# Kernel tuning notes

Hardware: AMD Instinct MI355X
Metric: run time of the kernel (lower is better)

The kernel has to match this reference:

```python
import jax, jax.numpy as jnp
import numpy as np

B, D_IN, D_H, D_OUT = 8192, 512, 256, 128
TEMP = 0.07
EPS_BN = 1e-5


def _bn(x, g, b):
    # BatchNorm1d in training mode: biased batch statistics
    mu = jnp.mean(x, axis=0)
    var = jnp.var(x, axis=0)
    return (x - mu) * jax.lax.rsqrt(var + EPS_BN) * g + b


def _project(x, W1, b1, g1, beta1, W2, b2, g2, beta2, W3, b3):
    h = jax.nn.relu(_bn(x @ W1 + b1, g1, beta1))
    h = jax.nn.relu(_bn(h @ W2 + b2, g2, beta2))
    return h @ W3 + b3  # (B, D_OUT)


def setup_inputs() -> dict:
    key = jax.random.key(0)
    ks = jax.random.split(key, 6)
    f32 = jnp.float32
    return {
        "x1": jax.random.normal(ks[0], (B, D_IN), f32),
        "x2": jax.random.normal(ks[1], (B, D_IN), f32),
        "W1": jax.random.normal(ks[2], (D_IN, D_H), f32) * 0.04,
        "b1": jnp.zeros((D_H,), f32),
        "g1": jnp.ones((D_H,), f32),
        "beta1": jnp.zeros((D_H,), f32),
        "W2": jax.random.normal(ks[3], (D_H, D_H), f32) * 0.06,
        "b2": jnp.zeros((D_H,), f32),
        "g2": jnp.ones((D_H,), f32),
        "beta2": jnp.zeros((D_H,), f32),
        "W3": jax.random.normal(ks[4], (D_H, D_OUT), f32) * 0.06,
        "b3": jnp.zeros((D_OUT,), f32),
    }


def reference(x1, x2, W1, b1, g1, beta1, W2, b2, g2, beta2, W3, b3):
    z1 = _project(x1, W1, b1, g1, beta1, W2, b2, g2, beta2, W3, b3)
    z2 = _project(x2, W1, b1, g1, beta1, W2, b2, g2, beta2, W3, b3)
    # F.normalize(dim=1), eps=1e-12
    z1 = z1 / jnp.maximum(jnp.linalg.norm(z1, axis=1, keepdims=True), 1e-12)
    z2 = z2 / jnp.maximum(jnp.linalg.norm(z2, axis=1, keepdims=True), 1e-12)
    reps = jnp.concatenate([z1, z2], axis=0)           # (2B, D)
    # cosine similarity of unit vectors == single GEMM (2B, 2B)
    sim = reps @ reps.T
    idx = jnp.arange(B)
    positives = jnp.concatenate([sim[idx, idx + B], sim[idx + B, idx]], axis=0)  # (2B,)
    nominator = jnp.exp(positives / TEMP)
    # source bug preserved: denominator sums sim/temp (no exp), masking the diagonal
    denominator = (jnp.sum(sim, axis=1) - jnp.diagonal(sim)) / TEMP
    loss = -jnp.log(nominator / denominator)
    return jnp.mean(loss)
```

## Files before the change

kernel.cpp:

```cpp
#include <hip/hip_runtime.h>
#include <math.h>

#define BATCH   8192
#define MROWS   16384
#define DIN     512
#define DH      256
#define DOUT    128
#define EPS_BN  1e-5f
#define TEMP    0.07f

using f4    = __attribute__((ext_vector_type(4))) float;
using f32x4 = __attribute__((ext_vector_type(4))) float;
using h4    = __attribute__((ext_vector_type(4))) _Float16;
using h8    = __attribute__((ext_vector_type(8))) _Float16;

#define GLD_LDS16(gp, lp) __builtin_amdgcn_global_load_lds( \
    (const __attribute__((address_space(1))) void*)(gp),    \
    (__attribute__((address_space(3))) void*)(lp), 16, 0, 0)


template <int K, int N, int EPI>
__global__ __launch_bounds__(256, 1) void gemm3h(
    const _Float16* __restrict__ Ahi, const _Float16* __restrict__ Alo,
    const _Float16* __restrict__ BThi, const _Float16* __restrict__ BTlo,
    const float* __restrict__ bias, float* __restrict__ Cout,
    float* __restrict__ red)
{
    constexpr int BM = 64, BN = 128;
    constexpr int NT = K / 64;
    constexpr int TA = 4096, TB = 8192;
    constexpr int BUF = 24576;

    __shared__ _Float16 ring[3][BUF];

    const int tid = threadIdx.x;
    const int wave = tid >> 6, lane = tid & 63;
    const int wr = wave >> 1, wc = wave & 1;
    const int l4 = lane >> 4, lc = lane & 15;
    const int brow = blockIdx.y * BM;
    const int bcol = blockIdx.x * BN;
    const size_t aT0 = (size_t)(brow >> 6) * NT;
    const size_t bT0 = (size_t)(bcol >> 7) * NT;

    const _Float16* srcb[12];
    int str[12];
#pragma unroll
    for (int i = 0; i < 12; ++i) {
        int c = wave * 12 + i;
        if (c < 8)       { srcb[i] = Ahi  + aT0 * TA + c * 512;        str[i] = TA; }
        else if (c < 16) { srcb[i] = Alo  + aT0 * TA + (c - 8) * 512;  str[i] = TA; }
        else if (c < 32) { srcb[i] = BThi + bT0 * TB + (c - 16) * 512; str[i] = TB; }
        else             { srcb[i] = BTlo + bT0 * TB + (c - 32) * 512; str[i] = TB; }
        srcb[i] += lane * 8;
    }

    auto stage = [&](int buf, int t) {
#pragma unroll
        for (int i = 0; i < 12; ++i)
            GLD_LDS16(srcb[i] + (size_t)t * str[i], &ring[buf][(wave * 12 + i) * 512]);
    };

    f32x4 acc[2][4];
#pragma unroll
    for (int mi = 0; mi < 2; ++mi)
#pragma unroll
        for (int ni = 0; ni < 4; ++ni)
#pragma unroll
            for (int c = 0; c < 4; ++c) acc[mi][ni][c] = 0.f;

    stage(0, 0);
    stage(1, 1);

#pragma unroll
    for (int t = 0; t < NT; ++t) {
        if (t < NT - 1) asm volatile("s_waitcnt vmcnt(12)" ::: "memory");
        else            asm volatile("s_waitcnt vmcnt(0)" ::: "memory");
        __builtin_amdgcn_s_barrier();
        __builtin_amdgcn_sched_barrier(0);
        const _Float16* L = ring[t % 3];
#pragma unroll
        for (int ks = 0; ks < 2; ++ks) {
            h8 ah[2], al[2], bh[4], bl[4];
#pragma unroll
            for (int mi = 0; mi < 2; ++mi) {
                int mf = wr * 2 + mi;
                ah[mi] = *(const h8*)&L[(mf * 2 + ks) * 512 + lane * 8];
                al[mi] = *(const h8*)&L[(8 + mf * 2 + ks) * 512 + lane * 8];
            }
#pragma unroll
            for (int ni = 0; ni < 4; ++ni) {
                int nf = wc * 4 + ni;
                bh[ni] = *(const h8*)&L[(16 + nf * 2 + ks) * 512 + lane * 8];
                bl[ni] = *(const h8*)&L[(32 + nf * 2 + ks) * 512 + lane * 8];
            }
#pragma unroll
            for (int mi = 0; mi < 2; ++mi)
#pragma unroll
                for (int ni = 0; ni < 4; ++ni) {
                    acc[mi][ni] = __builtin_amdgcn_mfma_f32_16x16x32_f16(
                        ah[mi], bh[ni], acc[mi][ni], 0, 0, 0);
                    acc[mi][ni] = __builtin_amdgcn_mfma_f32_16x16x32_f16(
                        al[mi], bh[ni], acc[mi][ni], 0, 0, 0);
                    acc[mi][ni] = __builtin_amdgcn_mfma_f32_16x16x32_f16(
                        ah[mi], bl[ni], acc[mi][ni], 0, 0, 0);
                }
        }
        if (t + 2 < NT) stage((t + 2) % 3, t + 2);
    }

    __syncthreads();
    float* sR = (float*)&ring[0][0];
    float* nL = (float*)((char*)sR + 8192);

    float bv[4];
#pragma unroll
    for (int ni = 0; ni < 4; ++ni) bv[ni] = bias[bcol + wc * 64 + ni * 16 + lc];

    if constexpr (EPI == 0) {
        const int half = (brow >= BATCH) ? 1 : 0;
        float s[4] = {}, q[4] = {};
#pragma unroll
        for (int mi = 0; mi < 2; ++mi)
#pragma unroll
            for (int j = 0; j < 4; ++j) {
                int gr = brow + wr * 32 + mi * 16 + l4 * 4 + j;
#pragma unroll
                for (int ni = 0; ni < 4; ++ni) {
                    float v = acc[mi][ni][j] + bv[ni];
                    Cout[(size_t)gr * N + bcol + wc * 64 + ni * 16 + lc] = v;
                    s[ni] += v;
                    q[ni] = fmaf(v, v, q[ni]);
                }
            }
#pragma unroll
        for (int ni = 0; ni < 4; ++ni) {
            sR[(wr * 4 + l4) * 128 + wc * 64 + ni * 16 + lc] = s[ni];
            sR[1024 + (wr * 4 + l4) * 128 + wc * 64 + ni * 16 + lc] = q[ni];
        }
        __syncthreads();
        if (tid < BN) {
            float ss = 0.f, qq = 0.f;
#pragma unroll
            for (int i = 0; i < 8; ++i) {
                ss += sR[i * 128 + tid];
                qq += sR[1024 + i * 128 + tid];
            }
            atomicAdd(&red[half * 512 + bcol + tid], ss);
            atomicAdd(&red[half * 512 + 256 + bcol + tid], qq);
        }
    } else {
        float v[2][4][4];
#pragma unroll
        for (int mi = 0; mi < 2; ++mi)
#pragma unroll
            for (int j = 0; j < 4; ++j) {
                float ssq = 0.f;
#pragma unroll
                for (int ni = 0; ni < 4; ++ni) {
                    v[mi][j][ni] = acc[mi][ni][j] + bv[ni];
                    ssq = fmaf(v[mi][j][ni], v[mi][j][ni], ssq);
                }
#pragma unroll
                for (int o = 1; o < 16; o <<= 1) ssq += __shfl_xor(ssq, o);
                if (lc == 0) nL[(wr * 32 + mi * 16 + l4 * 4 + j) * 2 + wc] = ssq;
            }
        __syncthreads();
        float s[4] = {};
#pragma unroll
        for (int mi = 0; mi < 2; ++mi)
#pragma unroll
            for (int j = 0; j < 4; ++j) {
                int lrow = wr * 32 + mi * 16 + l4 * 4 + j;
                float tot = nL[lrow * 2] + nL[lrow * 2 + 1];
                float inv = 1.0f / fmaxf(sqrtf(tot), 1e-12f);
#pragma unroll
                for (int ni = 0; ni < 4; ++ni) {
                    float z = v[mi][j][ni] * inv;
                    Cout[(size_t)(brow + lrow) * DOUT + wc * 64 + ni * 16 + lc] = z;
                    s[ni] += z;
                }
            }
        __syncthreads();
#pragma unroll
        for (int ni = 0; ni < 4; ++ni)
            sR[(wr * 4 + l4) * 128 + wc * 64 + ni * 16 + lc] = s[ni];
        __syncthreads();
        if (tid < BN) {
            float ss = 0.f;
#pragma unroll
            for (int i = 0; i < 8; ++i) ss += sR[i * 128 + tid];
            atomicAdd(&red[tid], ss);
        }
    }
}

__device__ __forceinline__ size_t tiledA(int r, int k, int KT) {
    return (size_t)((r >> 6) * KT + (k >> 6)) * 4096 +
           ((((r & 63) >> 4) * 2 + ((k & 63) >> 5)) * 512) +
           (((r & 15) | (((k & 31) >> 3) << 4)) * 8) + (k & 7);
}
__device__ __forceinline__ size_t tiledB(int n, int k, int KT) {
    return (size_t)((n >> 7) * KT + (k >> 6)) * 8192 +
           ((((n & 127) >> 4) * 2 + ((k & 63) >> 5)) * 512) +
           (((n & 15) | (((k & 31) >> 3) << 4)) * 8) + (k & 7);
}

__global__ __launch_bounds__(256) void split_xw(
    const float* __restrict__ x1, const float* __restrict__ x2,
    const float* __restrict__ W1, const float* __restrict__ W2,
    const float* __restrict__ W3,
    _Float16* __restrict__ Xhi, _Float16* __restrict__ Xlo,
    _Float16* __restrict__ W1hiT, _Float16* __restrict__ W1loT,
    _Float16* __restrict__ W2hiT, _Float16* __restrict__ W2loT,
    _Float16* __restrict__ W3hiT, _Float16* __restrict__ W3loT)
{
    const int b = blockIdx.x;
    if (b < 2048) {
        const float* src = (b < 1024) ? x1 : x2;
        const int rbase = (b < 1024) ? 0 : BATCH;
#pragma unroll
        for (int i = 0; i < 4; ++i) {
            size_t f = (size_t)(b & 1023) * 1024 + i * 256 + threadIdx.x;
            int r = rbase + (int)(f >> 7);
            int c0 = ((int)f & 127) << 2;
            f4 vv = ((const f4*)src)[f];
            h4 hi, lo;
#pragma unroll
            for (int j = 0; j < 4; ++j) {
                hi[j] = (_Float16)vv[j];
                lo[j] = (_Float16)(vv[j] - (float)hi[j]);
            }
            size_t d = tiledA(r, c0, DIN / 64);
            *(h4*)&Xhi[d] = hi;
            *(h4*)&Xlo[d] = lo;
        }
    } else {
        const int wb = b - 2048;
#pragma unroll
        for (int i = 0; i < 4; ++i) {
            int e = wb * 1024 + i * 256 + threadIdx.x;
            if (e < 131072) {
                int n = e >> 9, k = e & 511;
                float w = W1[(size_t)k * 256 + n];
                _Float16 hi = (_Float16)w;
                size_t d = tiledB(n, k, 8);
                W1hiT[d] = hi; W1loT[d] = (_Float16)(w - (float)hi);
            } else if (e < 196608) {
                int r = e - 131072;
                int n = r >> 8, k = r & 255;
                float w = W2[(size_t)k * 256 + n];
                _Float16 hi = (_Float16)w;
                size_t d = tiledB(n, k, 4);
                W2hiT[d] = hi; W2loT[d] = (_Float16)(w - (float)hi);
            } else {
                int r = e - 196608;
                int n = r >> 8, k = r & 255;
                float w = W3[(size_t)k * 128 + n];
                _Float16 hi = (_Float16)w;
                size_t d = tiledB(n, k, 4);
                W3hiT[d] = hi; W3loT[d] = (_Float16)(w - (float)hi);
            }
        }
    }
}

__global__ __launch_bounds__(256) void bnrelu_split(
    const float* __restrict__ Y, const float* __restrict__ stats,
    const float* __restrict__ g, const float* __restrict__ beta,
    _Float16* __restrict__ Hhi, _Float16* __restrict__ Hlo)
{
    const int c0 = (threadIdx.x & 63) << 2;
    const int rj = threadIdx.x >> 6;
    const int row0 = blockIdx.x * 64;
    const int half = (row0 >= BATCH) ? 1 : 0;
    const float invN = 1.0f / (float)BATCH;
    f4 sc, sh;
#pragma unroll
    for (int j = 0; j < 4; ++j) {
        int c = c0 + j;
        float mu = stats[half * 512 + c] * invN;
        float var = fmaf(-mu, mu, stats[half * 512 + 256 + c] * invN);
        float s = g[c] * rsqrtf(var + EPS_BN);
        sc[j] = s;
        sh[j] = fmaf(-mu, s, beta[c]);
    }
#pragma unroll 4
    for (int it = 0; it < 16; ++it) {
        int row = row0 + it * 4 + rj;
        f4 v = *(const f4*)(Y + (size_t)row * DH + c0);
        h4 hi, lo;
#pragma unroll
        for (int j = 0; j < 4; ++j) {
            float h = fmaxf(fmaf(v[j], sc[j], sh[j]), 0.f);
            hi[j] = (_Float16)h;
            lo[j] = (_Float16)(h - (float)hi[j]);
        }
        size_t d = tiledA(row, c0, DH / 64);
        *(h4*)&Hhi[d] = hi;
        *(h4*)&Hlo[d] = lo;
    }
}

__global__ __launch_bounds__(256) void losspos(const float* __restrict__ reps,
                                               const float* __restrict__ Svec,
                                               float* __restrict__ out)
{
    const int lane = threadIdx.x & 63;
    const int grp = threadIdx.x >> 6;
    __shared__ float part[4];
    float2 sv = ((const float2*)Svec)[lane];
    float acc = 0.f;
#pragma unroll 1
    for (int it = 0; it < 8; ++it) {
        int p = blockIdx.x * 32 + it * 4 + grp;
        float2 a = ((const float2*)(reps + (size_t)p * DOUT))[lane];
        float2 b = ((const float2*)(reps + (size_t)(p + BATCH) * DOUT))[lane];
        float dp  = fmaf(a.x, b.x, a.y * b.y);
        float rsA = fmaf(a.x, sv.x, a.y * sv.y);
        float sdA = fmaf(a.x, a.x, a.y * a.y);
        float rsB = fmaf(b.x, sv.x, b.y * sv.y);
        float sdB = fmaf(b.x, b.x, b.y * b.y);
#pragma unroll
        for (int o = 32; o; o >>= 1) {
            dp  += __shfl_xor(dp, o);
            rsA += __shfl_xor(rsA, o);
            sdA += __shfl_xor(sdA, o);
            rsB += __shfl_xor(rsB, o);
            sdB += __shfl_xor(sdB, o);
        }
        if (lane == 0) {
            float nom = expf(dp / TEMP);
            float dA = (rsA - sdA) / TEMP;
            float dB = (rsB - sdB) / TEMP;
            acc += -logf(nom / dA) - logf(nom / dB);
        }
    }
    if (lane == 0) part[grp] = acc;
    __syncthreads();
    if (threadIdx.x == 0) {
        float t = part[0] + part[1] + part[2] + part[3];
        atomicAdd(out, t * (1.0f / (float)MROWS));
    }
}

__global__ void zero_kernel(float* __restrict__ smalls, float* __restrict__ out)
{
    int i = blockIdx.x * 256 + threadIdx.x;
    if (i < 2176) smalls[i] = 0.f;
    if (i == 0) out[0] = 0.f;
}

extern "C" void kernel_launch(void* const* d_in, const int* in_sizes, int n_in,
                              void* d_out, int out_size, void* d_ws, size_t ws_size,
                              hipStream_t stream)
{
    const float* x1    = (const float*)d_in[0];
    const float* x2    = (const float*)d_in[1];
    const float* W1    = (const float*)d_in[2];
    const float* b1    = (const float*)d_in[3];
    const float* g1    = (const float*)d_in[4];
    const float* beta1 = (const float*)d_in[5];
    const float* W2    = (const float*)d_in[6];
    const float* b2    = (const float*)d_in[7];
    const float* g2    = (const float*)d_in[8];
    const float* beta2 = (const float*)d_in[9];
    const float* W3    = (const float*)d_in[10];
    const float* b3    = (const float*)d_in[11];
    float* out = (float*)d_out;

    char* W = (char*)d_ws;
    _Float16* XHI  = (_Float16*)(W);
    _Float16* XLO  = (_Float16*)(W + (16u << 20));
    float*    Y1   = (float*)   (W + (32u << 20));
    _Float16* H1HI = (_Float16*)(W);
    _Float16* H1LO = (_Float16*)(W + (8u << 20));
    float*    Y2   = (float*)   (W + (16u << 20));
    _Float16* H2HI = (_Float16*)(W);
    _Float16* H2LO = (_Float16*)(W + (8u << 20));
    float*    REPS = (float*)   (W + (16u << 20));
    char* wb = W + (48u << 20);
    _Float16* W1HIT = (_Float16*)(wb);
    _Float16* W1LOT = (_Float16*)(wb + 262144);
    _Float16* W2HIT = (_Float16*)(wb + 524288);
    _Float16* W2LOT = (_Float16*)(wb + 655360);
    _Float16* W3HIT = (_Float16*)(wb + 786432);
    _Float16* W3LOT = (_Float16*)(wb + 851968);
    float* smalls   = (float*)  (wb + 917504);
    float* stats1 = smalls;
    float* stats2 = smalls + 1024;
    float* Svec   = smalls + 2048;

    zero_kernel<<<9, 256, 0, stream>>>(smalls, out);

    split_xw<<<2272, 256, 0, stream>>>(x1, x2, W1, W2, W3, XHI, XLO,
                                       W1HIT, W1LOT, W2HIT, W2LOT, W3HIT, W3LOT);

    gemm3h<DIN, DH, 0><<<dim3(DH / 128, MROWS / 64), 256, 0, stream>>>(
        XHI, XLO, W1HIT, W1LOT, b1, Y1, stats1);
    bnrelu_split<<<MROWS / 64, 256, 0, stream>>>(Y1, stats1, g1, beta1, H1HI, H1LO);

    gemm3h<DH, DH, 0><<<dim3(DH / 128, MROWS / 64), 256, 0, stream>>>(
        H1HI, H1LO, W2HIT, W2LOT, b2, Y2, stats2);
    bnrelu_split<<<MROWS / 64, 256, 0, stream>>>(Y2, stats2, g2, beta2, H2HI, H2LO);

    gemm3h<DH, DOUT, 1><<<dim3(DOUT / 128, MROWS / 64), 256, 0, stream>>>(
        H2HI, H2LO, W3HIT, W3LOT, b3, REPS, Svec);

    losspos<<<BATCH / 32, 256, 0, stream>>>(REPS, Svec, out);
}
```

Before: 190.6 us.

## Fuse fp16 split and BatchNorm+ReLU into GEMM A-operand loading

The GEMM kernel now reads fp32 activations directly from global memory, applies the previous layer's BatchNorm scale/shift and ReLU in registers, and splits values into hi/lo fp16 before writing them to LDS. The standalone input split pass and the two bnrelu_split kernels go away, along with their tiled fp16 intermediate buffers. Weight prep and zeroing are merged into one small kernel. The K-step drops to 32 with a register-prefetched A path and launch bounds raised to 2 blocks per CU, which trades extra VALU conversion work inside the GEMM loop for less HBM traffic and fewer launches.

```diff
diff --git a/kernel.cpp b/kernel.cpp
--- a/kernel.cpp
+++ b/kernel.cpp
@@ -18,48 +18,87 @@
     (const __attribute__((address_space(1))) void*)(gp),    \
     (__attribute__((address_space(3))) void*)(lp), 16, 0, 0)
 
-
-template <int K, int N, int EPI>
-__global__ __launch_bounds__(256, 1) void gemm3h(
-    const _Float16* __restrict__ Ahi, const _Float16* __restrict__ Alo,
+template <int K, int N, int FUSE_BN, int EPI>
+__global__ __launch_bounds__(256, 2) void gemm_fused(
+    const float* __restrict__ A1, const float* __restrict__ A2, int splitRow,
     const _Float16* __restrict__ BThi, const _Float16* __restrict__ BTlo,
-    const float* __restrict__ bias, float* __restrict__ Cout,
-    float* __restrict__ red)
+    const float* __restrict__ stats, const float* __restrict__ g,
+    const float* __restrict__ beta, const float* __restrict__ bias,
+    float* __restrict__ Cout, float* __restrict__ red)
 {
-    constexpr int BM = 64, BN = 128;
-    constexpr int NT = K / 64;
-    constexpr int TA = 4096, TB = 8192;
-    constexpr int BUF = 24576;
-
-    __shared__ _Float16 ring[3][BUF];
+    constexpr int NT = K / 32;
 
     const int tid = threadIdx.x;
     const int wave = tid >> 6, lane = tid & 63;
     const int wr = wave >> 1, wc = wave & 1;
     const int l4 = lane >> 4, lc = lane & 15;
-    const int brow = blockIdx.y * BM;
-    const int bcol = blockIdx.x * BN;
-    const size_t aT0 = (size_t)(brow >> 6) * NT;
-    const size_t bT0 = (size_t)(bcol >> 7) * NT;
-
-    const _Float16* srcb[12];
-    int str[12];
-#pragma unroll
-    for (int i = 0; i < 12; ++i) {
-        int c = wave * 12 + i;
-        if (c < 8)       { srcb[i] = Ahi  + aT0 * TA + c * 512;        str[i] = TA; }
-        else if (c < 16) { srcb[i] = Alo  + aT0 * TA + (c - 8) * 512;  str[i] = TA; }
-        else if (c < 32) { srcb[i] = BThi + bT0 * TB + (c - 16) * 512; str[i] = TB; }
-        else             { srcb[i] = BTlo + bT0 * TB + (c - 32) * 512; str[i] = TB; }
-        srcb[i] += lane * 8;
-    }
-
-    auto stage = [&](int buf, int t) {
-#pragma unroll
-        for (int i = 0; i < 12; ++i)
-            GLD_LDS16(srcb[i] + (size_t)t * str[i], &ring[buf][(wave * 12 + i) * 512]);
+    const int wg = blockIdx.x;
+    const int brow = (wg & 255) * 64;
+    const int bcol = (wg >> 8) * 128;
+    const int half = (brow >= BATCH) ? 1 : 0;
+
+    __shared__ __align__(16) char smem[75776];
+    _Float16* Bring = (_Float16*)smem;
+    _Float16* Aring = (_Float16*)(smem + 49152);
+    float*    scsh  = (float*)(smem + 73728);
+    float*    sR    = (float*)(smem + 49152);
+    float*    nLp   = (float*)(smem + 49152 + 8192);
+
+    const _Float16* bsrc[4];
+    {
+        const int co = (bcol + wave * 32 + lc) * K + l4 * 8;
+        bsrc[0] = BThi + co;
+        bsrc[1] = BThi + co + 16 * K;
+        bsrc[2] = BTlo + co;
+        bsrc[3] = BTlo + co + 16 * K;
+    }
+    auto stageB = [&](int buf, int t) {
+        _Float16* d = Bring + buf * 8192 + wave * 1024;
+        GLD_LDS16(bsrc[0] + t * 32, d);
+        GLD_LDS16(bsrc[1] + t * 32, d + 512);
+        GLD_LDS16(bsrc[2] + t * 32, d + 4096);
+        GLD_LDS16(bsrc[3] + t * 32, d + 4096 + 512);
     };
 
+    const int arow = wave * 16 + lc;
+    const int ak0 = l4 * 8;
+    const int growA = brow + arow;
+    const float* asrc = (growA < splitRow)
+        ? (A1 + (size_t)growA * K + ak0)
+        : (A2 + (size_t)(growA - splitRow) * K + ak0);
+
+    f4 ar[2][2];
+    auto loadA = [&](int p, int t) {
+        ar[p][0] = *(const f4*)(asrc + t * 32);
+        ar[p][1] = *(const f4*)(asrc + t * 32 + 4);
+    };
+    auto procA = [&](int p, int buf, int t) {
+        float v[8];
+#pragma unroll
+        for (int j = 0; j < 4; ++j) { v[j] = ar[p][0][j]; v[4 + j] = ar[p][1][j]; }
+        if constexpr (FUSE_BN) {
+            f4 s0 = *(const f4*)&scsh[t * 32 + ak0];
+            f4 s1 = *(const f4*)&scsh[t * 32 + ak0 + 4];
+            f4 h0 = *(const f4*)&scsh[256 + t * 32 + ak0];
+            f4 h1 = *(const f4*)&scsh[256 + t * 32 + ak0 + 4];
+#pragma unroll
+            for (int j = 0; j < 4; ++j) {
+                v[j]     = fmaxf(fmaf(v[j],     s0[j], h0[j]), 0.f);
+                v[4 + j] = fmaxf(fmaf(v[4 + j], s1[j], h1[j]), 0.f);
+            }
+        }
+        h8 hi, lo;
+#pragma unroll
+        for (int j = 0; j < 8; ++j) {
+            _Float16 h = (_Float16)v[j];
+            hi[j] = h;
+            lo[j] = (_Float16)(v[j] - (float)h);
+        }
+        _Float16* d = Aring + buf * 4096 + wave * 512 + lane * 8;
+        *(h8*)d = hi;
+        *(h8*)(d + 2048) = lo;
+    };
+
     f32x4 acc[2][4];
 #pragma unroll
     for (int mi = 0; mi < 2; ++mi)
@@ -68,56 +107,75 @@
 #pragma unroll
             for (int c = 0; c < 4; ++c) acc[mi][ni][c] = 0.f;
 
-    stage(0, 0);
-    stage(1, 1);
+    auto compute = [&](int buf) {
+        const _Float16* Ab = Aring + buf * 4096;
+        const _Float16* Bb = Bring + buf * 8192;
+        h8 ah[2], al[2], bh[4], bl[4];
+#pragma unroll
+        for (int mi = 0; mi < 2; ++mi) {
+            ah[mi] = *(const h8*)(Ab + (wr * 2 + mi) * 512 + lane * 8);
+            al[mi] = *(const h8*)(Ab + 2048 + (wr * 2 + mi) * 512 + lane * 8);
+        }
+#pragma unroll
+        for (int ni = 0; ni < 4; ++ni) {
+            bh[ni] = *(const h8*)(Bb + (wc * 4 + ni) * 512 + lane * 8);
+            bl[ni] = *(const h8*)(Bb + 4096 + (wc * 4 + ni) * 512 + lane * 8);
+        }
+#pragma unroll
+        for (int mi = 0; mi < 2; ++mi)
+#pragma unroll
+            for (int ni = 0; ni < 4; ++ni) {
+                acc[mi][ni] = __builtin_amdgcn_mfma_f32_16x16x32_f16(
+                    ah[mi], bh[ni], acc[mi][ni], 0, 0, 0);
+                acc[mi][ni] = __builtin_amdgcn_mfma_f32_16x16x32_f16(
+                    al[mi], bh[ni], acc[mi][ni], 0, 0, 0);
+                acc[mi][ni] = __builtin_amdgcn_mfma_f32_16x16x32_f16(
+                    ah[mi], bl[ni], acc[mi][ni], 0, 0, 0);
+            }
+    };
+
+    if constexpr (FUSE_BN) {
+        const float invN = 1.0f / (float)BATCH;
+        float mu = stats[half * 512 + tid] * invN;
+        float var = fmaf(-mu, mu, stats[half * 512 + 256 + tid] * invN);
+        float s = g[tid] * rsqrtf(var + EPS_BN);
+        scsh[tid] = s;
+        scsh[256 + tid] = fmaf(-mu, s, beta[tid]);
+    }
+    loadA(0, 0);
+    stageB(0, 0);
+    stageB(1, 1);
+    if constexpr (FUSE_BN) {
+        asm volatile("s_waitcnt lgkmcnt(0)" ::: "memory");
+        __builtin_amdgcn_s_barrier();
+    }
+    procA(0, 0, 0);
+    loadA(1, 1);
+    asm volatile("s_waitcnt vmcnt(6)" ::: "memory");
+    asm volatile("s_waitcnt lgkmcnt(0)" ::: "memory");
+    __builtin_amdgcn_s_barrier();
 
 #pragma unroll
     for (int t = 0; t < NT; ++t) {
-        if (t < NT - 1) asm volatile("s_waitcnt vmcnt(12)" ::: "memory");
-        else            asm volatile("s_waitcnt vmcnt(0)" ::: "memory");
+        if (t + 2 < NT) stageB((t + 2) % 3, t + 2);
+        compute(t % 3);
+        if (t + 1 < NT) {
+            if (t + 2 < NT) asm volatile("s_waitcnt vmcnt(4)" ::: "memory");
+            else            asm volatile("s_waitcnt vmcnt(0)" ::: "memory");
+            __builtin_amdgcn_sched_barrier(0);
+            procA((t + 1) & 1, (t + 1) % 3, t + 1);
+            if (t + 2 < NT) loadA(t & 1, t + 2);
+        }
+        asm volatile("s_waitcnt lgkmcnt(0)" ::: "memory");
         __builtin_amdgcn_s_barrier();
-        __builtin_amdgcn_sched_barrier(0);
-        const _Float16* L = ring[t % 3];
-#pragma unroll
-        for (int ks = 0; ks < 2; ++ks) {
-            h8 ah[2], al[2], bh[4], bl[4];
-#pragma unroll
-            for (int mi = 0; mi < 2; ++mi) {
-                int mf = wr * 2 + mi;
-                ah[mi] = *(const h8*)&L[(mf * 2 + ks) * 512 + lane * 8];
-                al[mi] = *(const h8*)&L[(8 + mf * 2 + ks) * 512 + lane * 8];
-            }
-#pragma unroll
-            for (int ni = 0; ni < 4; ++ni) {
-                int nf = wc * 4 + ni;
-                bh[ni] = *(const h8*)&L[(16 + nf * 2 + ks) * 512 + lane * 8];
-                bl[ni] = *(const h8*)&L[(32 + nf * 2 + ks) * 512 + lane * 8];
-            }
-#pragma unroll
-            for (int mi = 0; mi < 2; ++mi)
-#pragma unroll
-                for (int ni = 0; ni < 4; ++ni) {
-                    acc[mi][ni] = __builtin_amdgcn_mfma_f32_16x16x32_f16(
-                        ah[mi], bh[ni], acc[mi][ni], 0, 0, 0);
-                    acc[mi][ni] = __builtin_amdgcn_mfma_f32_16x16x32_f16(
-                        al[mi], bh[ni], acc[mi][ni], 0, 0, 0);
-                    acc[mi][ni] = __builtin_amdgcn_mfma_f32_16x16x32_f16(
-                        ah[mi], bl[ni], acc[mi][ni], 0, 0, 0);
-                }
-        }
-        if (t + 2 < NT) stage((t + 2) % 3, t + 2);
-    }
-
+    }
     __syncthreads();
-    float* sR = (float*)&ring[0][0];
-    float* nL = (float*)((char*)sR + 8192);
 
     float bv[4];
 #pragma unroll
     for (int ni = 0; ni < 4; ++ni) bv[ni] = bias[bcol + wc * 64 + ni * 16 + lc];
 
     if constexpr (EPI == 0) {
-        const int half = (brow >= BATCH) ? 1 : 0;
         float s[4] = {}, q[4] = {};
 #pragma unroll
         for (int mi = 0; mi < 2; ++mi)
@@ -138,7 +196,7 @@
             sR[1024 + (wr * 4 + l4) * 128 + wc * 64 + ni * 16 + lc] = q[ni];
         }
         __syncthreads();
-        if (tid < BN) {
+        if (tid < 128) {
             float ss = 0.f, qq = 0.f;
 #pragma unroll
             for (int i = 0; i < 8; ++i) {
@@ -162,7 +220,7 @@
                 }
 #pragma unroll
                 for (int o = 1; o < 16; o <<= 1) ssq += __shfl_xor(ssq, o);
-                if (lc == 0) nL[(wr * 32 + mi * 16 + l4 * 4 + j) * 2 + wc] = ssq;
+                if (lc == 0) nLp[(wr * 32 + mi * 16 + l4 * 4 + j) * 2 + wc] = ssq;
             }
         __syncthreads();
         float s[4] = {};
@@ -171,7 +229,7 @@
 #pragma unroll
             for (int j = 0; j < 4; ++j) {
                 int lrow = wr * 32 + mi * 16 + l4 * 4 + j;
-                float tot = nL[lrow * 2] + nL[lrow * 2 + 1];
+                float tot = nLp[lrow * 2] + nLp[lrow * 2 + 1];
                 float inv = 1.0f / fmaxf(sqrtf(tot), 1e-12f);
 #pragma unroll
                 for (int ni = 0; ni < 4; ++ni) {
@@ -185,7 +243,7 @@
         for (int ni = 0; ni < 4; ++ni)
             sR[(wr * 4 + l4) * 128 + wc * 64 + ni * 16 + lc] = s[ni];
         __syncthreads();
-        if (tid < BN) {
+        if (tid < 128) {
             float ss = 0.f;
 #pragma unroll
             for (int i = 0; i < 8; ++i) ss += sR[i * 128 + tid];
@@ -194,110 +252,40 @@
     }
 }
 
-__device__ __forceinline__ size_t tiledA(int r, int k, int KT) {
-    return (size_t)((r >> 6) * KT + (k >> 6)) * 4096 +
-           ((((r & 63) >> 4) * 2 + ((k & 63) >> 5)) * 512) +
-           (((r & 15) | (((k & 31) >> 3) << 4)) * 8) + (k & 7);
-}
-__device__ __forceinline__ size_t tiledB(int n, int k, int KT) {
-    return (size_t)((n >> 7) * KT + (k >> 6)) * 8192 +
-           ((((n & 127) >> 4) * 2 + ((k & 63) >> 5)) * 512) +
-           (((n & 15) | (((k & 31) >> 3) << 4)) * 8) + (k & 7);
-}
-
-__global__ __launch_bounds__(256) void split_xw(
-    const float* __restrict__ x1, const float* __restrict__ x2,
+__global__ __launch_bounds__(256) void wprep(
     const float* __restrict__ W1, const float* __restrict__ W2,
     const float* __restrict__ W3,
-    _Float16* __restrict__ Xhi, _Float16* __restrict__ Xlo,
     _Float16* __restrict__ W1hiT, _Float16* __restrict__ W1loT,
     _Float16* __restrict__ W2hiT, _Float16* __restrict__ W2loT,
-    _Float16* __restrict__ W3hiT, _Float16* __restrict__ W3loT)
+    _Float16* __restrict__ W3hiT, _Float16* __restrict__ W3loT,
+    float* __restrict__ smalls, float* __restrict__ out)
 {
     const int b = blockIdx.x;
-    if (b < 2048) {
-        const float* src = (b < 1024) ? x1 : x2;
-        const int rbase = (b < 1024) ? 0 : BATCH;
-#pragma unroll
-        for (int i = 0; i < 4; ++i) {
-            size_t f = (size_t)(b & 1023) * 1024 + i * 256 + threadIdx.x;
-            int r = rbase + (int)(f >> 7);
-            int c0 = ((int)f & 127) << 2;
-            f4 vv = ((const f4*)src)[f];
-            h4 hi, lo;
-#pragma unroll
-            for (int j = 0; j < 4; ++j) {
-                hi[j] = (_Float16)vv[j];
-                lo[j] = (_Float16)(vv[j] - (float)hi[j]);
-            }
-            size_t d = tiledA(r, c0, DIN / 64);
-            *(h4*)&Xhi[d] = hi;
-            *(h4*)&Xlo[d] = lo;
-        }
-    } else {
-        const int wb = b - 2048;
-#pragma unroll
-        for (int i = 0; i < 4; ++i) {
-            int e = wb * 1024 + i * 256 + threadIdx.x;
-            if (e < 131072) {
-                int n = e >> 9, k = e & 511;
-                float w = W1[(size_t)k * 256 + n];
-                _Float16 hi = (_Float16)w;
-                size_t d = tiledB(n, k, 8);
-                W1hiT[d] = hi; W1loT[d] = (_Float16)(w - (float)hi);
-            } else if (e < 196608) {
-                int r = e - 131072;
-                int n = r >> 8, k = r & 255;
-                float w = W2[(size_t)k * 256 + n];
-                _Float16 hi = (_Float16)w;
-                size_t d = tiledB(n, k, 4);
-                W2hiT[d] = hi; W2loT[d] = (_Float16)(w - (float)hi);
-            } else {
-                int r = e - 196608;
-                int n = r >> 8, k = r & 255;
-                float w = W3[(size_t)k * 128 + n];
-                _Float16 hi = (_Float16)w;
-                size_t d = tiledB(n, k, 4);
-                W3hiT[d] = hi; W3loT[d] = (_Float16)(w - (float)hi);
-            }
-        }
-    }
-}
-
-__global__ __launch_bounds__(256) void bnrelu_split(
-    const float* __restrict__ Y, const float* __restrict__ stats,
-    const float* __restrict__ g, const float* __restrict__ beta,
-    _Float16* __restrict__ Hhi, _Float16* __restrict__ Hlo)
-{
-    const int c0 = (threadIdx.x & 63) << 2;
-    const int rj = threadIdx.x >> 6;
-    const int row0 = blockIdx.x * 64;
-    const int half = (row0 >= BATCH) ? 1 : 0;
-    const float invN = 1.0f / (float)BATCH;
-    f4 sc, sh;
-#pragma unroll
-    for (int j = 0; j < 4; ++j) {
-        int c = c0 + j;
-        float mu = stats[half * 512 + c] * invN;
-        float var = fmaf(-mu, mu, stats[half * 512 + 256 + c] * invN);
-        float s = g[c] * rsqrtf(var + EPS_BN);
-        sc[j] = s;
-        sh[j] = fmaf(-mu, s, beta[c]);
-    }
-#pragma unroll 4
-    for (int it = 0; it < 16; ++it) {
-        int row = row0 + it * 4 + rj;
-        f4 v = *(const f4*)(Y + (size_t)row * DH + c0);
+    if (b == 56) {
+        for (int i = threadIdx.x; i < 2176; i += 256) smalls[i] = 0.f;
+        if (threadIdx.x == 0) out[0] = 0.f;
+        return;
+    }
+#pragma unroll
+    for (int i = 0; i < 4; ++i) {
+        int qd = b * 1024 + i * 256 + threadIdx.x;
+        const float* src; _Float16 *dhi, *dlo; int n, kq, Nw, Kw;
+        if (qd < 32768)      { src = W1; dhi = W1hiT; dlo = W1loT;
+                               n = qd & 255;            kq = qd >> 8; Nw = 256; Kw = 512; }
+        else if (qd < 49152) { src = W2; dhi = W2hiT; dlo = W2loT;
+                               n = (qd - 32768) & 255;  kq = (qd - 32768) >> 8; Nw = 256; Kw = 256; }
+        else                 { src = W3; dhi = W3hiT; dlo = W3loT;
+                               n = (qd - 49152) & 127;  kq = (qd - 49152) >> 7; Nw = 128; Kw = 256; }
         h4 hi, lo;
 #pragma unroll
         for (int j = 0; j < 4; ++j) {
-            float h = fmaxf(fmaf(v[j], sc[j], sh[j]), 0.f);
-            hi[j] = (_Float16)h;
-            lo[j] = (_Float16)(h - (float)hi[j]);
-        }
-        size_t d = tiledA(row, c0, DH / 64);
-        *(h4*)&Hhi[d] = hi;
-        *(h4*)&Hlo[d] = lo;
+            float w = src[(size_t)(kq * 4 + j) * Nw + n];
+            _Float16 h = (_Float16)w;
+            hi[j] = h;
+            lo[j] = (_Float16)(w - (float)h);
+        }
+        *(h4*)&dhi[(size_t)n * Kw + kq * 4] = hi;
+        *(h4*)&dlo[(size_t)n * Kw + kq * 4] = lo;
     }
 }
 
@@ -343,13 +331,6 @@
     }
 }
 
-__global__ void zero_kernel(float* __restrict__ smalls, float* __restrict__ out)
-{
-    int i = blockIdx.x * 256 + threadIdx.x;
-    if (i < 2176) smalls[i] = 0.f;
-    if (i == 0) out[0] = 0.f;
-}
-
 extern "C" void kernel_launch(void* const* d_in, const int* in_sizes, int n_in,
                               void* d_out, int out_size, void* d_ws, size_t ws_size,
                               hipStream_t stream)
@@ -369,16 +350,10 @@
     float* out = (float*)d_out;
 
     char* W = (char*)d_ws;
-    _Float16* XHI  = (_Float16*)(W);
-    _Float16* XLO  = (_Float16*)(W + (16u << 20));
-    float*    Y1   = (float*)   (W + (32u << 20));
-    _Float16* H1HI = (_Float16*)(W);
-    _Float16* H1LO = (_Float16*)(W + (8u << 20));
-    float*    Y2   = (float*)   (W + (16u << 20));
-    _Float16* H2HI = (_Float16*)(W);
-    _Float16* H2LO = (_Float16*)(W + (8u << 20));
-    float*    REPS = (float*)   (W + (16u << 20));
-    char* wb = W + (48u << 20);
+    float*    Y1   = (float*)(W);
+    float*    Y2   = (float*)(W + (16u << 20));
+    float*    REPS = (float*)(W + (32u << 20));
+    char* wb = W + (40u << 20);
     _Float16* W1HIT = (_Float16*)(wb);
     _Float16* W1LOT = (_Float16*)(wb + 262144);
     _Float16* W2HIT = (_Float16*)(wb + 524288);
@@ -390,21 +365,19 @@
     float* stats2 = smalls + 1024;
     float* Svec   = smalls + 2048;
 
-    zero_kernel<<<9, 256, 0, stream>>>(smalls, out);
-
-    split_xw<<<2272, 256, 0, stream>>>(x1, x2, W1, W2, W3, XHI, XLO,
-                                       W1HIT, W1LOT, W2HIT, W2LOT, W3HIT, W3LOT);
-
-    gemm3h<DIN, DH, 0><<<dim3(DH / 128, MROWS / 64), 256, 0, stream>>>(
-        XHI, XLO, W1HIT, W1LOT, b1, Y1, stats1);
-    bnrelu_split<<<MROWS / 64, 256, 0, stream>>>(Y1, stats1, g1, beta1, H1HI, H1LO);
-
-    gemm3h<DH, DH, 0><<<dim3(DH / 128, MROWS / 64), 256, 0, stream>>>(
-        H1HI, H1LO, W2HIT, W2LOT, b2, Y2, stats2);
-    bnrelu_split<<<MROWS / 64, 256, 0, stream>>>(Y2, stats2, g2, beta2, H2HI, H2LO);
-
-    gemm3h<DH, DOUT, 1><<<dim3(DOUT / 128, MROWS / 64), 256, 0, stream>>>(
-        H2HI, H2LO, W3HIT, W3LOT, b3, REPS, Svec);
+    const int big = 1 << 30;
+
+    wprep<<<57, 256, 0, stream>>>(W1, W2, W3, W1HIT, W1LOT, W2HIT, W2LOT,
+                                  W3HIT, W3LOT, smalls, out);
+
+    gemm_fused<DIN, DH, 0, 0><<<512, 256, 0, stream>>>(
+        x1, x2, BATCH, W1HIT, W1LOT, nullptr, nullptr, nullptr, b1, Y1, stats1);
+
+    gemm_fused<DH, DH, 1, 0><<<512, 256, 0, stream>>>(
+        Y1, Y1, big, W2HIT, W2LOT, stats1, g1, beta1, b2, Y2, stats2);
+
+    gemm_fused<DH, DOUT, 1, 1><<<256, 256, 0, stream>>>(
+        Y2, Y2, big, W3HIT, W3LOT, stats2, g2, beta2, b3, REPS, Svec);
 
     losspos<<<BATCH / 32, 256, 0, stream>>>(REPS, Svec, out);
 }
```

Measured after the change: 166.7 us. 12.5% less time.
